# Kernel tuning notes

Measured on AMD Instinct MI355X. Metric: run time of the kernel, lower is better.

## Reference

```python
import math
import jax, jax.numpy as jnp
import numpy as np

EPS = 1e-6

def rmsnorm(x, g):
    # RMSNorm: x / rms(x) * g
    return x * jax.lax.rsqrt(jnp.mean(x * x, axis=-1, keepdims=True) + EPS) * g

def setup_inputs() -> dict:
    key = jax.random.key(0)
    ks = jax.random.split(key, 10)
    B, S, D, H = 1, 4096, 1024, 16
    dh = D // H
    s = 0.02  # init scale for weights
    x = jax.random.normal(ks[0], (B, S, D), dtype=jnp.float32)
    # causal mask: masked_fill(mask == 0, -inf) => lower-triangular ones
    mask = jnp.tril(jnp.ones((S, S), dtype=jnp.int32))
    WQ = jax.random.normal(ks[1], (H, D, dh), dtype=jnp.float32) * s
    WK = jax.random.normal(ks[2], (H, D, dh), dtype=jnp.float32) * s
    WV = jax.random.normal(ks[3], (H, D, dh), dtype=jnp.float32) * s
    WO = jax.random.normal(ks[4], (D, D), dtype=jnp.float32) * s
    W1 = jax.random.normal(ks[5], (D, 4 * D), dtype=jnp.float32) * s
    B1 = jnp.zeros((4 * D,), dtype=jnp.float32)
    W2 = jax.random.normal(ks[6], (4 * D, D), dtype=jnp.float32) * s
    B2 = jnp.zeros((D,), dtype=jnp.float32)
    g1 = jnp.ones((D,), dtype=jnp.float32)
    g2 = jnp.ones((D,), dtype=jnp.float32)
    return {"x": x, "mask": mask, "g1": g1, "WQ": WQ, "WK": WK, "WV": WV,
            "WO": WO, "g2": g2, "W1": W1, "B1": B1, "W2": W2, "B2": B2}

def reference(x, mask, g1, WQ, WK, WV, WO, g2, W1, B1, W2, B2):
    dh = WQ.shape[-1]
    # --- attention sub-block (pre-norm) ---
    h = rmsnorm(x, g1)                                   # [B,S,D]
    Q = jnp.einsum('bsd,hde->bhse', h, WQ)               # [B,H,S,dh]
    K = jnp.einsum('bsd,hde->bhse', h, WK)
    V = jnp.einsum('bsd,hde->bhse', h, WV)
    # rope() in the source is identity
    scores = jnp.einsum('bhse,bhte->bhst', Q, K) / math.sqrt(dh)  # [B,H,S,S]
    scores = jnp.where(mask == 0, -jnp.inf, scores)
    attn = jax.nn.softmax(scores, axis=-1)
    o = jnp.einsum('bhst,bhte->bhse', attn, V)           # [B,H,S,dh]
    Bn, H, S, e = o.shape
    o = o.transpose(0, 2, 1, 3).reshape(Bn, S, H * e)    # concat heads on last dim
    x = x + o @ WO
    # --- MLP sub-block (pre-norm) ---
    h2 = rmsnorm(x, g2)
    m = jax.nn.relu(h2 @ W1 + B1) @ W2 + B2
    return x + m
```

## Files before the change

### kernel.cpp

```cpp
#include <hip/hip_runtime.h>
#include <hip/hip_bf16.h>

typedef __attribute__((ext_vector_type(8))) short bf16x8;
typedef __attribute__((ext_vector_type(4))) float f32x4;
typedef __attribute__((ext_vector_type(4))) short s16x4;

#define GLOBAL_AS(p) ((const __attribute__((address_space(1))) void*)(p))
#define LDS_AS(p)    ((__attribute__((address_space(3))) void*)(p))

__device__ __forceinline__ short f2bf(float f) {
  return __builtin_bit_cast(short, __float2bfloat16(f));
}
__device__ __forceinline__ float bf2f(short s) {
  return __bfloat162float(__builtin_bit_cast(__hip_bfloat16, s));
}

__global__ __launch_bounds__(256) void prep_kernel(
    const float* __restrict__ WQ, const float* __restrict__ WK,
    const float* __restrict__ WV, short* __restrict__ wqkv_t,
    const float* __restrict__ WO, short* __restrict__ wo_t,
    const float* __restrict__ W1, short* __restrict__ w1_t,
    const float* __restrict__ W2, short* __restrict__ w2_t) {
  __shared__ short Ls[64][66];
  const int tid = threadIdx.x;
  const int l = tid & 63, q4 = tid >> 6;
  const int bid = blockIdx.x;

  if (bid < 768) {
    const int x = bid & 15, y = bid >> 4;
    const int hh = y & 15, proj = y >> 4;
    const float* W = (proj == 0) ? WQ : ((proj == 1) ? WK : WV);
    const float scl = (proj == 0) ? 0.125f : 1.f;
    const int d0 = x * 64;
#pragma unroll
    for (int rep = 0; rep < 16; ++rep) {
      int dd = q4 * 16 + rep;
      Ls[dd][l] = f2bf(W[(size_t)hh * 65536 + (size_t)(d0 + dd) * 64 + l] * scl);
    }
    __syncthreads();
#pragma unroll
    for (int rep = 0; rep < 16; ++rep) {
      int ee = q4 * 16 + rep;
      wqkv_t[(size_t)(proj * 1024 + hh * 64 + ee) * 1024 + d0 + l] = Ls[l][ee];
    }
  } else {
    const float* in; short* out; int R, C, bx, by;
    if (bid < 1024) {
      int idx = bid - 768;  in = WO; out = wo_t; R = 1024; C = 1024;
      bx = idx & 15; by = idx >> 4;
    } else if (bid < 2048) {
      int idx = bid - 1024; in = W1; out = w1_t; R = 1024; C = 4096;
      bx = idx & 63; by = idx >> 6;
    } else {
      int idx = bid - 2048; in = W2; out = w2_t; R = 4096; C = 1024;
      bx = idx & 15; by = idx >> 4;
    }
    const int c0 = bx * 64, r0 = by * 64;
#pragma unroll
    for (int rep = 0; rep < 16; ++rep) {
      int rr = q4 * 16 + rep;
      Ls[rr][l] = f2bf(in[(size_t)(r0 + rr) * C + c0 + l]);
    }
    __syncthreads();
#pragma unroll
    for (int rep = 0; rep < 16; ++rep) {
      int cc = q4 * 16 + rep;
      out[(size_t)(c0 + cc) * R + r0 + l] = Ls[l][cc];
    }
  }
}

__global__ __launch_bounds__(256) void transpose_v_kernel(
    const short* __restrict__ qkv, short* __restrict__ vt, int S) {
  __shared__ short Ls[64][66];
  const int tid = threadIdx.x;
  const int l = tid & 63, q4 = tid >> 6;
  const int s0 = blockIdx.x * 64, e0 = blockIdx.y * 64;
#pragma unroll
  for (int rep = 0; rep < 16; ++rep) {
    int rr = q4 * 16 + rep;
    Ls[rr][l] = qkv[(size_t)(s0 + rr) * 3072 + 2048 + e0 + l];
  }
  __syncthreads();
#pragma unroll
  for (int rep = 0; rep < 16; ++rep) {
    int ee = q4 * 16 + rep;
    vt[(size_t)(e0 + ee) * S + s0 + l] = Ls[l][ee];
  }
}

__global__ __launch_bounds__(256) void rmsnorm_kernel(
    const float* __restrict__ x, const float* __restrict__ g,
    short* __restrict__ out, int D) {
  const int row = blockIdx.x;
  const int tid = threadIdx.x;
  const float4 xv = *(const float4*)&x[(size_t)row * D + tid * 4];
  float ss = xv.x * xv.x + xv.y * xv.y + xv.z * xv.z + xv.w * xv.w;
#pragma unroll
  for (int off = 32; off; off >>= 1) ss += __shfl_xor(ss, off);
  __shared__ float red[4];
  if ((tid & 63) == 0) red[tid >> 6] = ss;
  __syncthreads();
  float tot = red[0] + red[1] + red[2] + red[3];
  float scale = rsqrtf(tot / (float)D + 1e-6f);
  const float4 gv = *(const float4*)&g[tid * 4];
  s16x4 o;
  o[0] = f2bf(xv.x * scale * gv.x);
  o[1] = f2bf(xv.y * scale * gv.y);
  o[2] = f2bf(xv.z * scale * gv.z);
  o[3] = f2bf(xv.w * scale * gv.w);
  *(s16x4*)&out[(size_t)row * D + tid * 4] = o;
}

__global__ __launch_bounds__(256) void gemm_bt64_kernel(
    const short* __restrict__ A, const short* __restrict__ BT,
    int M, int N, int K,
    float* __restrict__ outF, const float* __restrict__ addend) {
  __shared__ short As[128 * 32];
  __shared__ short Bs[64 * 32];
  const int tid = threadIdx.x;
  const int lane = tid & 63;
  const int wid = tid >> 6;
  const int lrow = lane & 15;
  const int kk = lane >> 4;
  const int row0 = blockIdx.y * 128;
  const int col0 = blockIdx.x * 64;
  const int wm = wid >> 1, wn = wid & 1;

  f32x4 acc[4][2] = {};

  for (int k0 = 0; k0 < K; k0 += 32) {
    __syncthreads();
#pragma unroll
    for (int it = 0; it < 2; ++it) {
      int c = it * 256 + tid;
      int r = c >> 2, c8 = (c & 3) * 8;
      const short* ga = A + (size_t)(row0 + r) * K + k0 + c8;
      short* la = &As[(size_t)(it * 256 + wid * 64) * 8];
      __builtin_amdgcn_global_load_lds(GLOBAL_AS(ga), LDS_AS(la), 16, 0, 0);
    }
    {
      int r = tid >> 2, c8 = (tid & 3) * 8;
      const short* gb = BT + (size_t)(col0 + r) * K + k0 + c8;
      short* lb = &Bs[(size_t)(wid * 64) * 8];
      __builtin_amdgcn_global_load_lds(GLOBAL_AS(gb), LDS_AS(lb), 16, 0, 0);
    }
    __syncthreads();

    bf16x8 a[4], b[2];
#pragma unroll
    for (int i = 0; i < 4; ++i)
      a[i] = *(const bf16x8*)&As[(wm * 64 + i * 16 + lrow) * 32 + kk * 8];
#pragma unroll
    for (int j = 0; j < 2; ++j)
      b[j] = *(const bf16x8*)&Bs[(wn * 32 + j * 16 + lrow) * 32 + kk * 8];
#pragma unroll
    for (int i = 0; i < 4; ++i)
#pragma unroll
      for (int j = 0; j < 2; ++j)
        acc[i][j] = __builtin_amdgcn_mfma_f32_16x16x32_bf16(a[i], b[j], acc[i][j], 0, 0, 0);
  }

#pragma unroll
  for (int i = 0; i < 4; ++i) {
    int row = row0 + wm * 64 + i * 16 + kk * 4;
#pragma unroll
    for (int j = 0; j < 2; ++j) {
      int col = col0 + wn * 32 + j * 16 + lrow;
#pragma unroll
      for (int r = 0; r < 4; ++r) {
        size_t o = (size_t)(row + r) * N + col;
        outF[o] = acc[i][j][r] + addend[o];
      }
    }
  }
}

#define READ_A(buf, mh)                                                      \
  _Pragma("unroll") for (int m4 = 0; m4 < 4; ++m4) {                         \
    int row_ = wm * 128 + ((mh)*4 + m4) * 16 + lrow;                         \
    _Pragma("unroll") for (int k_ = 0; k_ < 2; ++k_) {                       \
      int sl_ = (k_ * 4 + kk) ^ (row_ & 7);                                  \
      aA[m4][k_] = *(const bf16x8*)&lds[buf][0][row_ * 64 + sl_ * 8];        \
    }                                                                        \
  }
#define READ_B2(buf, pr)                                                     \
  _Pragma("unroll") for (int nn = 0; nn < 2; ++nn) {                         \
    int n_ = (pr)*2 + nn;                                                    \
    int row_ = wn * 64 + n_ * 16 + lrow;                                     \
    _Pragma("unroll") for (int k_ = 0; k_ < 2; ++k_) {                       \
      int sl_ = (k_ * 4 + kk) ^ (row_ & 7);                                  \
      bB[n_][k_] = *(const bf16x8*)&lds[buf][1][row_ * 64 + sl_ * 8];        \
    }                                                                        \
  }
#define MFMA16(mh, nh)                                                       \
  _Pragma("unroll") for (int m4 = 0; m4 < 4; ++m4)                           \
  _Pragma("unroll") for (int n2 = 0; n2 < 2; ++n2)                           \
  _Pragma("unroll") for (int k_ = 0; k_ < 2; ++k_)                           \
    acc[(mh)*4 + m4][(nh)*2 + n2] = __builtin_amdgcn_mfma_f32_16x16x32_bf16( \
        aA[m4][k_], bB[(nh)*2 + n2][k_], acc[(mh)*4 + m4][(nh)*2 + n2], 0, 0, 0);
#define STAGE_HALF(buf, mat, half, kt)                                       \
  {                                                                          \
    const short* g_ = ((mat) ? Bb : Ab) + (size_t)((half)*128) * K + (kt)*64;\
    short* l_ = &lds[buf][mat][(half)*8192];                                 \
    _Pragma("unroll") for (int it_ = 0; it_ < 2; ++it_) {                    \
      int ci_ = it_ * 512 + tid;                                             \
      int r_ = ci_ >> 3, sl_ = (ci_ & 7) ^ (r_ & 7);                         \
      __builtin_amdgcn_global_load_lds(GLOBAL_AS(g_ + (size_t)r_ * K + sl_ * 8), \
                                       LDS_AS(l_ + ci_ * 8), 16, 0, 0);      \
    }                                                                        \
  }
#define PH_SYNC1()                                                           \
  __builtin_amdgcn_s_barrier();                                              \
  asm volatile("s_waitcnt lgkmcnt(0)" ::: "memory");                         \
  __builtin_amdgcn_sched_barrier(0);                                         \
  __builtin_amdgcn_s_setprio(1)
#define PH_SYNC2()                                                           \
  __builtin_amdgcn_s_setprio(0);                                             \
  __builtin_amdgcn_s_barrier()
#define PH_SYNC2_VM(n)                                                       \
  __builtin_amdgcn_s_setprio(0);                                             \
  asm volatile("s_waitcnt vmcnt(" #n ")" ::: "memory");                      \
  __builtin_amdgcn_s_barrier()

template <int EPI>
__global__ __launch_bounds__(512, 2) void gemm256_kernel(
    const short* __restrict__ A, const short* __restrict__ BT,
    int N, int K, int kslice, size_t pstride,
    short* __restrict__ outB, const float* __restrict__ bias) {
  __shared__ short lds[2][2][16384];
  const int tid = threadIdx.x;
  const int lane = tid & 63, wid = tid >> 6;
  const int lrow = lane & 15, kk = lane >> 4;
  const int wm = wid >> 2, wn = wid & 3;
  const int row0 = blockIdx.y * 256, col0 = blockIdx.x * 256;
  const int kbase = blockIdx.z * kslice;
  const int NT = kslice >> 6;

  const short* Ab = A + (size_t)row0 * K + kbase;
  const short* Bb = BT + (size_t)col0 * K + kbase;

  f32x4 acc[8][4] = {};
  bf16x8 aA[4][2], bB[4][2];

  STAGE_HALF(0, 1, 0, 0); STAGE_HALF(0, 0, 0, 0);
  STAGE_HALF(0, 1, 1, 0); STAGE_HALF(0, 0, 1, 0);
  STAGE_HALF(1, 1, 0, 1); STAGE_HALF(1, 0, 0, 1); STAGE_HALF(1, 0, 1, 1);
  asm volatile("s_waitcnt vmcnt(6)" ::: "memory");
  __builtin_amdgcn_s_barrier();

  const int iters = NT >> 1;
  for (int i = 0; i < iters; ++i) {
    const int t1 = 2 * i + 1;
    int kt2 = 2 * i + 2; if (kt2 >= NT) kt2 -= NT;
    int kt3 = 2 * i + 3; if (kt3 >= NT) kt3 -= NT;
    READ_A(0, 0); READ_B2(0, 0); STAGE_HALF(1, 1, 1, t1);
    PH_SYNC1(); MFMA16(0, 0); PH_SYNC2();
    READ_B2(0, 1);
    PH_SYNC1(); MFMA16(0, 1); PH_SYNC2();
    READ_A(0, 1); STAGE_HALF(0, 1, 0, kt2);
    PH_SYNC1(); MFMA16(1, 0); PH_SYNC2();
    STAGE_HALF(0, 0, 0, kt2);
    PH_SYNC1(); MFMA16(1, 1); PH_SYNC2_VM(4);
    READ_A(1, 0); READ_B2(1, 0); STAGE_HALF(0, 1, 1, kt2);
    PH_SYNC1(); MFMA16(0, 0); PH_SYNC2();
    READ_B2(1, 1); STAGE_HALF(0, 0, 1, kt2);
    PH_SYNC1(); MFMA16(0, 1); PH_SYNC2();
    READ_A(1, 1); STAGE_HALF(1, 1, 0, kt3);
    PH_SYNC1(); MFMA16(1, 0); PH_SYNC2();
    STAGE_HALF(1, 0, 0, kt3); STAGE_HALF(1, 0, 1, kt3);
    PH_SYNC1(); MFMA16(1, 1); PH_SYNC2_VM(6);
  }

  short* ob = outB + (size_t)blockIdx.z * pstride;
#pragma unroll
  for (int m = 0; m < 8; ++m) {
    int row = row0 + wm * 128 + m * 16 + kk * 4;
#pragma unroll
    for (int n = 0; n < 4; ++n) {
      int col = col0 + wn * 64 + n * 16 + lrow;
#pragma unroll
      for (int r = 0; r < 4; ++r) {
        float v = acc[m][n][r];
        size_t o = (size_t)(row + r) * N + col;
        if (EPI == 0) {
          ob[o] = f2bf(v);
        } else {
          v += bias[col];
          ob[o] = f2bf(v > 0.f ? v : 0.f);
        }
      }
    }
  }
}

__global__ __launch_bounds__(256) void reduce4_kernel(
    const short* __restrict__ part, const float* __restrict__ bias,
    const float* __restrict__ addend, float* __restrict__ out) {
  const size_t MN = (size_t)4096 * 1024;
  size_t i8 = ((size_t)blockIdx.x * 256 + threadIdx.x) * 8;
  bf16x8 p0 = *(const bf16x8*)&part[i8];
  bf16x8 p1 = *(const bf16x8*)&part[MN + i8];
  bf16x8 p2 = *(const bf16x8*)&part[2 * MN + i8];
  bf16x8 p3 = *(const bf16x8*)&part[3 * MN + i8];
  int col = (int)(i8 & 1023);
#pragma unroll
  for (int j = 0; j < 8; ++j) {
    float v = (bf2f(p0[j]) + bf2f(p1[j])) + (bf2f(p2[j]) + bf2f(p3[j]));
    out[i8 + j] = v + bias[col + j] + addend[i8 + j];
  }
}

__device__ const unsigned char QT_SLOT[48] = {
    31, 31, 30, 15, 30, 29, 29, 28, 14, 28, 27, 27, 26, 13, 26, 25,
    25, 24, 12, 24, 23, 23, 22, 11, 22, 21, 21, 20, 10, 20, 19, 19,
    18,  9, 18, 17, 17, 16,  8, 16,  7,  6,  5,  4,  3,  2,  1,  0};
__device__ const unsigned char SP_SLOT[48] = {
    0, 1, 0, 0, 1, 0, 1, 0, 0, 1, 0, 1, 0, 0, 1, 0,
    1, 0, 0, 1, 0, 1, 0, 0, 1, 0, 1, 0, 0, 1, 0, 1,
    0, 0, 1, 0, 1, 0, 0, 1, 0, 0, 0, 0, 0, 0, 0, 0};

__global__ __launch_bounds__(512, 6) void attn_kernel(
    const short* __restrict__ QKV, const short* __restrict__ VT,
    float* __restrict__ opart, float* __restrict__ lpart,
    short* __restrict__ O) {
  const int S = 4096;
  __shared__ short Ks[2][64 * 64];
  __shared__ short Vs[2][64 * 64];
  __shared__ short Ps[8][16 * 64];

  const int tid = threadIdx.x;
  const int lane = tid & 63;
  const int w = tid >> 6;
  const int lrow = lane & 15;
  const int kk = lane >> 4;
  const int bid = blockIdx.x;
  const int h = bid & 15;
  const int slot = bid >> 4;
  const int qtile = QT_SLOT[slot];
  const int sp = SP_SLOT[slot];
  const int T = 2 * qtile + 2;
  const bool split = (qtile >= 16);
  const int half = qtile + 1;
  const int t0 = (split && sp) ? half : 0;
  const int t1 = (split && !sp) ? half : T;
  const int q0 = qtile * 128;
  const int qw = q0 + w * 16;
  const int myq = qw + lrow;

  auto stage = [&](int buf, int t) {
    const int kv0 = t * 64;
    int krow = tid >> 3;
    int ksl = (tid & 7) ^ (krow & 7);
    const short* gk = QKV + (size_t)(kv0 + krow) * 3072 + 1024 + h * 64 + ksl * 8;
    const short* gv = VT + (size_t)(h * 64 + krow) * S + kv0 + ksl * 8;
    __builtin_amdgcn_global_load_lds(GLOBAL_AS(gk),
                                     LDS_AS(&Ks[buf][(w * 64) * 8]), 16, 0, 0);
    __builtin_amdgcn_global_load_lds(GLOBAL_AS(gv),
                                     LDS_AS(&Vs[buf][(w * 64) * 8]), 16, 0, 0);
  };

  bf16x8 qf[2];
#pragma unroll
  for (int half2 = 0; half2 < 2; ++half2)
    qf[half2] = *(const bf16x8*)&QKV[(size_t)(qw + lrow) * 3072 +
                                     h * 64 + half2 * 32 + kk * 8];

  float rs_acc = 0.f;
  f32x4 o_acc[4] = {};

  stage(0, t0);
  __syncthreads();
  int cur = 0;

  for (int t = t0; t < t1; ++t) {
    if (t + 1 < t1) stage(cur ^ 1, t + 1);

    const int kvc = t * 64;
    if (kvc <= qw + 15) {
      bf16x8 kf[4][2];
#pragma unroll
      for (int c = 0; c < 4; ++c)
#pragma unroll
        for (int half2 = 0; half2 < 2; ++half2) {
          int krow = c * 16 + lrow;
          kf[c][half2] = *(const bf16x8*)&Ks[cur][krow * 64 + (((half2 * 4 + kk) ^ (krow & 7)) * 8)];
        }
      f32x4 sc[4];
      __builtin_amdgcn_s_setprio(1);
#pragma unroll
      for (int c = 0; c < 4; ++c) {
        f32x4 z = {};
        z = __builtin_amdgcn_mfma_f32_16x16x32_bf16(kf[c][0], qf[0], z, 0, 0, 0);
        z = __builtin_amdgcn_mfma_f32_16x16x32_bf16(kf[c][1], qf[1], z, 0, 0, 0);
        sc[c] = z;
      }
      __builtin_amdgcn_s_setprio(0);

      if (kvc + 63 <= qw) {
#pragma unroll
        for (int c = 0; c < 4; ++c) {
          float p0 = __expf(sc[c][0]), p1 = __expf(sc[c][1]);
          float p2 = __expf(sc[c][2]), p3 = __expf(sc[c][3]);
          rs_acc += (p0 + p1) + (p2 + p3);
          s16x4 pk;
          pk[0] = f2bf(p0); pk[1] = f2bf(p1); pk[2] = f2bf(p2); pk[3] = f2bf(p3);
          int slot8 = c * 2 + (kk >> 1);
          *(s16x4*)&Ps[w][lrow * 64 + ((slot8 ^ (lrow & 7)) * 8) + (kk & 1) * 4] = pk;
        }
      } else {
#pragma unroll
        for (int c = 0; c < 4; ++c) {
          const int keyb = kvc + c * 16 + kk * 4;
          float pv[4];
#pragma unroll
          for (int r = 0; r < 4; ++r) {
            float p = __expf(sc[c][r]);
            if (keyb + r > myq) p = 0.f;
            pv[r] = p;
          }
          rs_acc += (pv[0] + pv[1]) + (pv[2] + pv[3]);
          s16x4 pk;
          pk[0] = f2bf(pv[0]); pk[1] = f2bf(pv[1]); pk[2] = f2bf(pv[2]); pk[3] = f2bf(pv[3]);
          int slot8 = c * 2 + (kk >> 1);
          *(s16x4*)&Ps[w][lrow * 64 + ((slot8 ^ (lrow & 7)) * 8) + (kk & 1) * 4] = pk;
        }
      }

#pragma unroll
      for (int ks = 0; ks < 2; ++ks) {
        bf16x8 pf2, vf[4];
        {
          int qrow = lrow;
          pf2 = *(const bf16x8*)&Ps[w][qrow * 64 + (((ks * 4 + kk) ^ (qrow & 7)) * 8)];
        }
#pragma unroll
        for (int g = 0; g < 4; ++g) {
          int erow = g * 16 + lrow;
          vf[g] = *(const bf16x8*)&Vs[cur][erow * 64 + (((ks * 4 + kk) ^ (erow & 7)) * 8)];
        }
        __builtin_amdgcn_s_setprio(1);
#pragma unroll
        for (int g = 0; g < 4; ++g)
          o_acc[g] = __builtin_amdgcn_mfma_f32_16x16x32_bf16(pf2, vf[g], o_acc[g], 0, 0, 0);
        __builtin_amdgcn_s_setprio(0);
      }
    }

    __syncthreads();
    cur ^= 1;
  }

  float l = rs_acc;
  l += __shfl_xor(l, 16);
  l += __shfl_xor(l, 32);

  if (!split) {
    float inv_[4];
#pragma unroll
    for (int r = 0; r < 4; ++r) inv_[r] = 1.f / __shfl(l, kk * 4 + r);
#pragma unroll
    for (int g = 0; g < 4; ++g)
#pragma unroll
      for (int r = 0; r < 4; ++r) {
        int s_idx = qw + kk * 4 + r;
        O[(size_t)s_idx * 1024 + h * 64 + g * 16 + lrow] =
            f2bf(o_acc[g][r] * inv_[r]);
      }
  } else {
    const int pidx = (h * 32 + qtile) * 2 + sp;
    float* op = opart + (size_t)pidx * 8192;
    float* lp = lpart + pidx * 128;
    if (lane < 16) lp[w * 16 + lrow] = l;
#pragma unroll
    for (int g = 0; g < 4; ++g)
#pragma unroll
      for (int r = 0; r < 4; ++r)
        op[(w * 16 + kk * 4 + r) * 64 + g * 16 + lrow] = o_acc[g][r];
  }
}

__global__ __launch_bounds__(256) void attn_combine_kernel(
    const float* __restrict__ opart, const float* __restrict__ lpart,
    short* __restrict__ O) {
  size_t e8 = ((size_t)blockIdx.x * 256 + threadIdx.x) * 8 + (size_t)2048 * 1024;
  const int srow = (int)(e8 >> 10);
  const int col = (int)(e8 & 1023);
  const int h = col >> 6, d = col & 63;
  const int qtile = srow >> 7, qr = srow & 127;
  const int pb = (h * 32 + qtile) * 2;
  const float* o0 = opart + (size_t)pb * 8192 + qr * 64 + d;
  const float* o1 = opart + (size_t)(pb + 1) * 8192 + qr * 64 + d;
  float l = lpart[pb * 128 + qr] + lpart[(pb + 1) * 128 + qr];
  float4 a0 = *(const float4*)o0;
  float4 a1 = *(const float4*)(o0 + 4);
  float4 b0 = *(const float4*)o1;
  float4 b1 = *(const float4*)(o1 + 4);
  a0.x += b0.x; a0.y += b0.y; a0.z += b0.z; a0.w += b0.w;
  a1.x += b1.x; a1.y += b1.y; a1.z += b1.z; a1.w += b1.w;
  float inv = 1.f / l;
  bf16x8 o;
  o[0] = f2bf(a0.x * inv); o[1] = f2bf(a0.y * inv);
  o[2] = f2bf(a0.z * inv); o[3] = f2bf(a0.w * inv);
  o[4] = f2bf(a1.x * inv); o[5] = f2bf(a1.y * inv);
  o[6] = f2bf(a1.z * inv); o[7] = f2bf(a1.w * inv);
  *(bf16x8*)&O[e8] = o;
}

extern "C" void kernel_launch(void* const* d_in, const int* in_sizes, int n_in,
                              void* d_out, int out_size, void* d_ws, size_t ws_size,
                              hipStream_t stream) {
  const float* x  = (const float*)d_in[0];
  const float* g1 = (const float*)d_in[2];
  const float* WQ = (const float*)d_in[3];
  const float* WK = (const float*)d_in[4];
  const float* WV = (const float*)d_in[5];
  const float* WO = (const float*)d_in[6];
  const float* g2 = (const float*)d_in[7];
  const float* W1 = (const float*)d_in[8];
  const float* B1 = (const float*)d_in[9];
  const float* W2 = (const float*)d_in[10];
  const float* B2 = (const float*)d_in[11];
  float* out = (float*)d_out;

  const int S = 4096, D = 1024, H = 16;

  char* ws = (char*)d_ws;
  size_t off = 0;
  auto alloc = [&](size_t bytes) -> void* {
    void* p = ws + off;
    off += (bytes + 255) & ~(size_t)255;
    return p;
  };
  short* h1     = (short*)alloc((size_t)S * D * 2);
  short* wqkv_t = (short*)alloc((size_t)3072 * 1024 * 2);
  short* qkv    = (short*)alloc((size_t)S * 3072 * 2);
  short* vt     = (short*)alloc((size_t)1024 * S * 2);
  short* attn_o = (short*)alloc((size_t)S * D * 2);
  short* wo_t   = (short*)alloc((size_t)1024 * 1024 * 2);
  float* x2     = (float*)alloc((size_t)S * D * 4);
  short* h2     = (short*)alloc((size_t)S * D * 2);
  short* w1_t   = (short*)alloc((size_t)4096 * 1024 * 2);
  short* m1     = (short*)alloc((size_t)S * 4096 * 2);
  short* w2_t   = (short*)alloc((size_t)1024 * 4096 * 2);
  short* partW2 = qkv;
  float* opart  = (float*)m1;
  float* lpart  = (float*)h1;

  prep_kernel<<<dim3(3072), 256, 0, stream>>>(WQ, WK, WV, wqkv_t,
                                              WO, wo_t, W1, w1_t, W2, w2_t);

  rmsnorm_kernel<<<S, 256, 0, stream>>>(x, g1, h1, D);
  gemm256_kernel<0><<<dim3(3072 / 256, S / 256, 1), 512, 0, stream>>>(
      h1, wqkv_t, 3072, 1024, 1024, 0, qkv, nullptr);
  transpose_v_kernel<<<dim3(S / 64, 1024 / 64), 256, 0, stream>>>(qkv, vt, S);
  attn_kernel<<<dim3(768), 512, 0, stream>>>(qkv, vt, opart, lpart, attn_o);
  attn_combine_kernel<<<dim3((2048 * 1024 / 8) / 256), 256, 0, stream>>>(opart, lpart, attn_o);
  gemm_bt64_kernel<<<dim3(1024 / 64, S / 128), 256, 0, stream>>>(
      attn_o, wo_t, S, 1024, 1024, x2, x);

  rmsnorm_kernel<<<S, 256, 0, stream>>>(x2, g2, h2, D);
  gemm256_kernel<2><<<dim3(4096 / 256, 4096 / 256, 1), 512, 0, stream>>>(
      h2, w1_t, 4096, 1024, 1024, 0, m1, B1);
  gemm256_kernel<0><<<dim3(1024 / 256, 4096 / 256, 4), 512, 0, stream>>>(
      m1, w2_t, 1024, 4096, 1024, (size_t)4096 * 1024, partW2, nullptr);
  reduce4_kernel<<<2048, 256, 0, stream>>>(partW2, B2, x2, out);
}
```

Baseline: 231.8 us.

## Fuse first RMSNorm into prep kernel and pass attention P via shuffles

```diff
diff --git a/kernel.cpp b/kernel.cpp
--- a/kernel.cpp
+++ b/kernel.cpp
@@ -4,6 +4,7 @@
 typedef __attribute__((ext_vector_type(8))) short bf16x8;
 typedef __attribute__((ext_vector_type(4))) float f32x4;
 typedef __attribute__((ext_vector_type(4))) short s16x4;
+typedef __attribute__((ext_vector_type(4))) unsigned u32x4;
 
 #define GLOBAL_AS(p) ((const __attribute__((address_space(1))) void*)(p))
 #define LDS_AS(p)    ((__attribute__((address_space(3))) void*)(p))
@@ -13,6 +14,9 @@
 }
 __device__ __forceinline__ float bf2f(short s) {
   return __bfloat162float(__builtin_bit_cast(__hip_bfloat16, s));
+}
+__device__ __forceinline__ unsigned packbf(float a, float b) {
+  return (unsigned)(unsigned short)f2bf(a) | ((unsigned)(unsigned short)f2bf(b) << 16);
 }
 
 __global__ __launch_bounds__(256) void prep_kernel(
@@ -20,18 +24,41 @@
     const float* __restrict__ WV, short* __restrict__ wqkv_t,
     const float* __restrict__ WO, short* __restrict__ wo_t,
     const float* __restrict__ W1, short* __restrict__ w1_t,
-    const float* __restrict__ W2, short* __restrict__ w2_t) {
+    const float* __restrict__ W2, short* __restrict__ w2_t,
+    const float* __restrict__ x, const float* __restrict__ g1,
+    short* __restrict__ h1) {
   __shared__ short Ls[64][66];
+  __shared__ float red[4];
   const int tid = threadIdx.x;
   const int l = tid & 63, q4 = tid >> 6;
   const int bid = blockIdx.x;
 
+  if (bid >= 3072) {
+    const int row = bid - 3072;
+    const float4 xv = *(const float4*)&x[(size_t)row * 1024 + tid * 4];
+    float ss = xv.x * xv.x + xv.y * xv.y + xv.z * xv.z + xv.w * xv.w;
+#pragma unroll
+    for (int off = 32; off; off >>= 1) ss += __shfl_xor(ss, off);
+    if ((tid & 63) == 0) red[tid >> 6] = ss;
+    __syncthreads();
+    float tot = red[0] + red[1] + red[2] + red[3];
+    float scale = rsqrtf(tot / 1024.f + 1e-6f);
+    const float4 gv = *(const float4*)&g1[tid * 4];
+    s16x4 o;
+    o[0] = f2bf(xv.x * scale * gv.x);
+    o[1] = f2bf(xv.y * scale * gv.y);
+    o[2] = f2bf(xv.z * scale * gv.z);
+    o[3] = f2bf(xv.w * scale * gv.w);
+    *(s16x4*)&h1[(size_t)row * 1024 + tid * 4] = o;
+    return;
+  }
+
   if (bid < 768) {
-    const int x = bid & 15, y = bid >> 4;
+    const int xb = bid & 15, y = bid >> 4;
     const int hh = y & 15, proj = y >> 4;
     const float* W = (proj == 0) ? WQ : ((proj == 1) ? WK : WV);
     const float scl = (proj == 0) ? 0.125f : 1.f;
-    const int d0 = x * 64;
+    const int d0 = xb * 64;
 #pragma unroll
     for (int rep = 0; rep < 16; ++rep) {
       int dd = q4 * 16 + rep;
@@ -320,14 +347,13 @@
     1, 0, 0, 1, 0, 1, 0, 0, 1, 0, 1, 0, 0, 1, 0, 1,
     0, 0, 1, 0, 1, 0, 0, 1, 0, 0, 0, 0, 0, 0, 0, 0};
 
-__global__ __launch_bounds__(512, 6) void attn_kernel(
+__global__ __launch_bounds__(512, 8) void attn_kernel(
     const short* __restrict__ QKV, const short* __restrict__ VT,
     float* __restrict__ opart, float* __restrict__ lpart,
     short* __restrict__ O) {
   const int S = 4096;
   __shared__ short Ks[2][64 * 64];
   __shared__ short Vs[2][64 * 64];
-  __shared__ short Ps[8][16 * 64];
 
   const int tid = threadIdx.x;
   const int lane = tid & 63;
@@ -347,6 +373,9 @@
   const int q0 = qtile * 128;
   const int qw = q0 + w * 16;
   const int myq = qw + lrow;
+  const int srcA = ((kk & 1) << 5) + lrow;
+  const int srcB = srcA + 16;
+  const bool hiC = (kk >> 1) != 0;
 
   auto stage = [&](int buf, int t) {
     const int kv0 = t * 64;
@@ -397,16 +426,15 @@
       }
       __builtin_amdgcn_s_setprio(0);
 
+      unsigned pd[4][2];
       if (kvc + 63 <= qw) {
 #pragma unroll
         for (int c = 0; c < 4; ++c) {
           float p0 = __expf(sc[c][0]), p1 = __expf(sc[c][1]);
           float p2 = __expf(sc[c][2]), p3 = __expf(sc[c][3]);
           rs_acc += (p0 + p1) + (p2 + p3);
-          s16x4 pk;
-          pk[0] = f2bf(p0); pk[1] = f2bf(p1); pk[2] = f2bf(p2); pk[3] = f2bf(p3);
-          int slot8 = c * 2 + (kk >> 1);
-          *(s16x4*)&Ps[w][lrow * 64 + ((slot8 ^ (lrow & 7)) * 8) + (kk & 1) * 4] = pk;
+          pd[c][0] = packbf(p0, p1);
+          pd[c][1] = packbf(p2, p3);
         }
       } else {
 #pragma unroll
@@ -420,20 +448,28 @@
             pv[r] = p;
           }
           rs_acc += (pv[0] + pv[1]) + (pv[2] + pv[3]);
-          s16x4 pk;
-          pk[0] = f2bf(pv[0]); pk[1] = f2bf(pv[1]); pk[2] = f2bf(pv[2]); pk[3] = f2bf(pv[3]);
-          int slot8 = c * 2 + (kk >> 1);
-          *(s16x4*)&Ps[w][lrow * 64 + ((slot8 ^ (lrow & 7)) * 8) + (kk & 1) * 4] = pk;
+          pd[c][0] = packbf(pv[0], pv[1]);
+          pd[c][1] = packbf(pv[2], pv[3]);
         }
       }
 
 #pragma unroll
       for (int ks = 0; ks < 2; ++ks) {
-        bf16x8 pf2, vf[4];
-        {
-          int qrow = lrow;
-          pf2 = *(const bf16x8*)&Ps[w][qrow * 64 + (((ks * 4 + kk) ^ (qrow & 7)) * 8)];
-        }
+        unsigned a0 = __shfl((int)pd[ks * 2][0], srcA);
+        unsigned b0 = __shfl((int)pd[ks * 2 + 1][0], srcA);
+        unsigned a1 = __shfl((int)pd[ks * 2][1], srcA);
+        unsigned b1 = __shfl((int)pd[ks * 2 + 1][1], srcA);
+        unsigned a2 = __shfl((int)pd[ks * 2][0], srcB);
+        unsigned b2 = __shfl((int)pd[ks * 2 + 1][0], srcB);
+        unsigned a3 = __shfl((int)pd[ks * 2][1], srcB);
+        unsigned b3 = __shfl((int)pd[ks * 2 + 1][1], srcB);
+        u32x4 pw;
+        pw[0] = hiC ? b0 : a0;
+        pw[1] = hiC ? b1 : a1;
+        pw[2] = hiC ? b2 : a2;
+        pw[3] = hiC ? b3 : a3;
+        bf16x8 pf2 = __builtin_bit_cast(bf16x8, pw);
+        bf16x8 vf[4];
 #pragma unroll
         for (int g = 0; g < 4; ++g) {
           int erow = g * 16 + lrow;
@@ -547,10 +583,10 @@
   float* opart  = (float*)m1;
   float* lpart  = (float*)h1;
 
-  prep_kernel<<<dim3(3072), 256, 0, stream>>>(WQ, WK, WV, wqkv_t,
-                                              WO, wo_t, W1, w1_t, W2, w2_t);
-
-  rmsnorm_kernel<<<S, 256, 0, stream>>>(x, g1, h1, D);
+  prep_kernel<<<dim3(3072 + S), 256, 0, stream>>>(WQ, WK, WV, wqkv_t,
+                                                  WO, wo_t, W1, w1_t, W2, w2_t,
+                                                  x, g1, h1);
+
   gemm256_kernel<0><<<dim3(3072 / 256, S / 256, 1), 512, 0, stream>>>(
       h1, wqkv_t, 3072, 1024, 1024, 0, qkv, nullptr);
   transpose_v_kernel<<<dim3(S / 64, 1024 / 64), 256, 0, stream>>>(qkv, vt, S);
```

Result: slower. 253.2 us (+9.3%).
